# Performance work log

Measured on AMD Instinct MI355X. Metric: run time of the kernel, lower is better.

Reference implementation:

```python
import jax, jax.numpy as jnp
import numpy as np

N_MEMORY = 16
FEA_DIM = 512


def setup_inputs() -> dict:
    key = jax.random.key(0)
    ks = jax.random.split(key, 8)
    b, L, d, n = 4, 4096, FEA_DIM, N_MEMORY
    scale = 1.0 / np.sqrt(d)  # ~ torch Linear default init scale
    return {
        "query": jax.random.normal(ks[0], (b, L, d), dtype=jnp.float32),
        "W1": jax.random.uniform(ks[1], (n, d, d), jnp.float32, -scale, scale),
        "b1": jax.random.uniform(ks[2], (n, d), jnp.float32, -scale, scale),
        "W2": jax.random.uniform(ks[3], (n, d, d), jnp.float32, -scale, scale),
        "b2": jax.random.uniform(ks[4], (n, d), jnp.float32, -scale, scale),
        "Wg": jax.random.uniform(ks[5], (n, d), jnp.float32, -scale, scale),
        "bg": jax.random.uniform(ks[6], (n,), jnp.float32, -scale, scale),
        "topk": 8,
    }


def reference(query, W1, b1, W2, b2, Wg, bg, topk):
    # query: [b, L, d]; stacked per-memory-slot params: W1/W2 [n, d, d], Wg [n, d]
    n = W1.shape[0]
    # per-slot LeakyReLU negative slopes: 0.01 + 0.2/n * l
    slopes = (0.01 + 0.2 / n * jnp.arange(n, dtype=query.dtype))[:, None, None, None]
    # memory_function: Linear -> LeakyReLU(slope_l) -> Linear -> Tanh, all slots at once
    h = jnp.einsum('bld,ndh->nblh', query, W1) + b1[:, None, None, :]   # [n,b,L,d]
    h = jnp.where(h >= 0, h, h * slopes)
    x = jnp.tanh(jnp.einsum('nblh,nhd->nbld', h, W2) + b2[:, None, None, :])  # [n,b,L,d]
    # gate: Linear(d,1) -> softmax over L -> topk over L -> gather -> weighted sum
    logits = jnp.einsum('nbld,nd->nbl', x, Wg) + bg[:, None, None]      # [n,b,L]
    w = jax.nn.softmax(logits, axis=-1)
    top_w, top_idx = jax.lax.top_k(w, topk)                             # [n,b,k]
    items = jnp.take_along_axis(x, top_idx[..., None], axis=2)          # [n,b,k,d]
    combined = jnp.einsum('nbkd,nbk->nbd', items, top_w)                # [n,b,d]
    m_item = jnp.transpose(combined, (1, 0, 2))                         # [b,n,d]
    # F.normalize(dim=-1), eps=1e-12
    norm = jnp.maximum(jnp.linalg.norm(m_item, axis=-1, keepdims=True), 1e-12)
    return m_item / norm
```

## Files before the change

kernel.cpp:

```cpp
#include <hip/hip_runtime.h>
#include <hip/hip_bf16.h>
#include <cstdint>
#include <cstddef>

#define NMEM 16
#define DDIM 512
#define BATCH 4
#define LSEQ 4096
#define ROWS 16384
#define NCAND 32
#define KTOP 8
#define QPAD 20

typedef __attribute__((ext_vector_type(4))) float f32x4;
typedef __attribute__((ext_vector_type(16))) float f32x16;
typedef __attribute__((ext_vector_type(8))) int int8v;

__device__ inline void gld16(const void* gptr, void* lptr) {
    __builtin_amdgcn_global_load_lds(
        (const __attribute__((address_space(1))) unsigned int*)gptr,
        (__attribute__((address_space(3))) unsigned int*)lptr,
        16, 0, 0);
}

__device__ inline float fast_tanh(float p) {
    p = fminf(fmaxf(p, -15.f), 15.f);
    float e = __expf(2.f * p);
    return (e - 1.f) / (e + 1.f);
}

__device__ inline int8v load_frag(const unsigned char* Ts, int row, int g, int hs) {
    int h = (row >> hs) & 7;
    const int4* p0 = (const int4*)(Ts + row * 128 + (((2 * g) ^ h) << 4));
    const int4* p1 = (const int4*)(Ts + row * 128 + (((2 * g + 1) ^ h) << 4));
    int4 x = *p0, y = *p1;
    int8v v;
    v[0] = x.x; v[1] = x.y; v[2] = x.z; v[3] = x.w;
    v[4] = y.x; v[5] = y.y; v[6] = y.z; v[7] = y.w;
    return v;
}

__global__ __launch_bounds__(256)
void prep_kernel(const float* __restrict__ query,
                 const float* __restrict__ W1, const float* __restrict__ W2,
                 unsigned char* __restrict__ Q8,
                 unsigned char* __restrict__ W1T8, unsigned char* __restrict__ W2T8,
                 float* __restrict__ logits) {
    int blk = blockIdx.x, t = threadIdx.x;
    if (blk < 2048) {
        size_t base = ((size_t)blk * 256 + t) * 16;
        const float4* in = (const float4*)(query + base);
        int4 o; int* op = (int*)&o;
        #pragma unroll
        for (int q = 0; q < 4; ++q) {
            float4 v = in[q];
            int lo = __builtin_amdgcn_cvt_pk_fp8_f32(v.x, v.y, 0, false);
            op[q] = __builtin_amdgcn_cvt_pk_fp8_f32(v.z, v.w, lo, true);
        }
        *(int4*)(Q8 + base) = o;
    } else if (blk < 4096) {
        __shared__ float tile[64][69];
        int bid = blk - 2048;
        const float* Win = W1; unsigned char* Wout = W1T8;
        if (bid >= 1024) { bid -= 1024; Win = W2; Wout = W2T8; }
        int n = bid >> 6, t64 = bid & 63;
        int dt = (t64 >> 3) << 6, jt = (t64 & 7) << 6;
        const float* inN = Win + (size_t)n * DDIM * DDIM;
        unsigned char* outN = Wout + (size_t)n * DDIM * DDIM;
        int rr = t >> 4, cc = (t & 15) * 4;
        #pragma unroll
        for (int pass = 0; pass < 4; ++pass) {
            int row = rr + pass * 16;
            float4 v = *(const float4*)(inN + (size_t)(dt + row) * DDIM + jt + cc);
            tile[row][cc] = v.x; tile[row][cc + 1] = v.y;
            tile[row][cc + 2] = v.z; tile[row][cc + 3] = v.w;
        }
        __syncthreads();
        #pragma unroll
        for (int pass = 0; pass < 4; ++pass) {
            int jl = rr + pass * 16;
            float f0 = tile[cc][jl], f1 = tile[cc + 1][jl];
            float f2 = tile[cc + 2][jl], f3 = tile[cc + 3][jl];
            int lo = __builtin_amdgcn_cvt_pk_fp8_f32(f0, f1, 0, false);
            int dw = __builtin_amdgcn_cvt_pk_fp8_f32(f2, f3, lo, true);
            *(int*)(outN + (size_t)(jt + jl) * DDIM + dt + cc) = dw;
        }
    } else {
        int bid = blk - 4096;
        ((int4*)logits)[bid * 256 + t] = int4{0, 0, 0, 0};
    }
}

__global__ __launch_bounds__(256, 2)
void fused_mlp_kernel(const unsigned char* __restrict__ Q8,
                      const unsigned char* __restrict__ W1T8,
                      const unsigned char* __restrict__ W2T8,
                      const float* __restrict__ b1, const float* __restrict__ b2,
                      const float* __restrict__ Wg,
                      float* __restrict__ logits)
{
    __shared__ unsigned char hbuf[128 * 512];
    __shared__ unsigned char Bs[128 * 128];
    const int id = blockIdx.x;
    const int n = id & 15;
    const int m0 = (id >> 4) * 128;
    const int tid = threadIdx.x, lane = tid & 63, w = tid >> 6;
    const int rh = w >> 1, ch = w & 1;
    const int l31 = lane & 31, kh = lane >> 5;
    const unsigned char* W1n = W1T8 + (size_t)n * DDIM * DDIM;
    const unsigned char* W2n = W2T8 + (size_t)n * DDIM * DDIM;
    const float slope = 0.01f + 0.0125f * n;
    const unsigned char* Aq0 = Q8 + (size_t)(m0 + rh * 64 + l31) * DDIM + kh * 32;

    for (int n0 = 0; n0 < 4; ++n0) {
        f32x16 acc[2][2] = {};
        const unsigned char* Bg = W1n + (size_t)(n0 * 128) * DDIM;
        for (int kt = 0; kt < 4; ++kt) {
            int8v av[2][2];
            #pragma unroll
            for (int rt = 0; rt < 2; ++rt)
                #pragma unroll
                for (int ks = 0; ks < 2; ++ks) {
                    const unsigned char* ap = Aq0 + (size_t)rt * 32 * DDIM + kt * 128 + ks * 64;
                    int4 x = *(const int4*)ap;
                    int4 y = *(const int4*)(ap + 16);
                    av[rt][ks][0] = x.x; av[rt][ks][1] = x.y;
                    av[rt][ks][2] = x.z; av[rt][ks][3] = x.w;
                    av[rt][ks][4] = y.x; av[rt][ks][5] = y.y;
                    av[rt][ks][6] = y.z; av[rt][ks][7] = y.w;
                }
            #pragma unroll
            for (int i = 0; i < 4; ++i) {
                int c = i * 256 + tid;
                int row = c >> 3, chk = c & 7;
                gld16(Bg + (size_t)row * DDIM + kt * 128 + ((chk ^ (row & 7)) << 4),
                      &Bs[c * 16]);
            }
            __syncthreads();
            #pragma unroll
            for (int ks = 0; ks < 2; ++ks)
                #pragma unroll
                for (int fc = 0; fc < 2; ++fc) {
                    int8v bfr = load_frag(Bs, ch * 64 + fc * 32 + l31, ks * 2 + kh, 0);
                    #pragma unroll
                    for (int rt = 0; rt < 2; ++rt)
                        acc[rt][fc] = __builtin_amdgcn_mfma_scale_f32_32x32x64_f8f6f4(
                            av[rt][ks], bfr, acc[rt][fc], 0, 0, 0,
                            0x7F7F7F7F, 0, 0x7F7F7F7F);
                }
            __syncthreads();
        }
        #pragma unroll
        for (int fc = 0; fc < 2; ++fc) {
            int D = n0 * 128 + ch * 64 + fc * 32 + l31;
            float bias = b1[n * DDIM + D];
            #pragma unroll
            for (int rt = 0; rt < 2; ++rt)
                #pragma unroll
                for (int reg = 0; reg < 16; ++reg) {
                    int row = rh * 64 + rt * 32 + (reg & 3) + 8 * (reg >> 2) + 4 * kh;
                    float v = acc[rt][fc][reg] + bias;
                    v = v >= 0.f ? v : v * slope;
                    int pk = __builtin_amdgcn_cvt_pk_fp8_f32(v, v, 0, false);
                    hbuf[row * 512 + (((D >> 4) ^ (row & 7)) << 4) + (D & 15)]
                        = (unsigned char)(pk & 0xff);
                }
        }
    }

    float rowacc[2][16] = {};
    for (int n0 = 0; n0 < 4; ++n0) {
        f32x16 acc[2][2] = {};
        const unsigned char* Bg = W2n + (size_t)(n0 * 128) * DDIM;
        for (int kt = 0; kt < 4; ++kt) {
            #pragma unroll
            for (int i = 0; i < 4; ++i) {
                int c = i * 256 + tid;
                int row = c >> 3, chk = c & 7;
                gld16(Bg + (size_t)row * DDIM + kt * 128 + ((chk ^ (row & 7)) << 4),
                      &Bs[c * 16]);
            }
            __syncthreads();
            #pragma unroll
            for (int ks = 0; ks < 2; ++ks) {
                int8v av[2];
                #pragma unroll
                for (int rt = 0; rt < 2; ++rt) {
                    int hrow = rh * 64 + rt * 32 + l31, hq = hrow & 7;
                    int C0 = kt * 8 + ks * 4 + 2 * kh;
                    const int4* p0 = (const int4*)(hbuf + hrow * 512 + ((C0 ^ hq) << 4));
                    const int4* p1 = (const int4*)(hbuf + hrow * 512 + (((C0 + 1) ^ hq) << 4));
                    int4 x = *p0, y = *p1;
                    av[rt][0] = x.x; av[rt][1] = x.y; av[rt][2] = x.z; av[rt][3] = x.w;
                    av[rt][4] = y.x; av[rt][5] = y.y; av[rt][6] = y.z; av[rt][7] = y.w;
                }
                #pragma unroll
                for (int fc = 0; fc < 2; ++fc) {
                    int8v bfr = load_frag(Bs, ch * 64 + fc * 32 + l31, ks * 2 + kh, 0);
                    #pragma unroll
                    for (int rt = 0; rt < 2; ++rt)
                        acc[rt][fc] = __builtin_amdgcn_mfma_scale_f32_32x32x64_f8f6f4(
                            av[rt], bfr, acc[rt][fc], 0, 0, 0,
                            0x7F7F7F7F, 0, 0x7F7F7F7F);
                }
            }
            __syncthreads();
        }
        #pragma unroll
        for (int fc = 0; fc < 2; ++fc) {
            int j = n0 * 128 + ch * 64 + fc * 32 + l31;
            float bias = b2[n * DDIM + j];
            float wgv = Wg[n * DDIM + j];
            #pragma unroll
            for (int rt = 0; rt < 2; ++rt)
                #pragma unroll
                for (int reg = 0; reg < 16; ++reg)
                    rowacc[rt][reg] = fmaf(fast_tanh(acc[rt][fc][reg] + bias), wgv,
                                           rowacc[rt][reg]);
        }
    }
    #pragma unroll
    for (int sh = 1; sh < 32; sh <<= 1)
        #pragma unroll
        for (int rt = 0; rt < 2; ++rt)
            #pragma unroll
            for (int reg = 0; reg < 16; ++reg)
                rowacc[rt][reg] += __shfl_xor(rowacc[rt][reg], sh);
    if (l31 == 0) {
        float* Ln = logits + (size_t)n * ROWS + m0 + rh * 64 + 4 * kh;
        #pragma unroll
        for (int rt = 0; rt < 2; ++rt)
            #pragma unroll
            for (int reg = 0; reg < 16; ++reg)
                atomicAdd(&Ln[rt * 32 + (reg & 3) + 8 * (reg >> 2)], rowacc[rt][reg]);
    }
}

__global__ __launch_bounds__(256)
void topcand_kernel(const float* __restrict__ logits, int* __restrict__ cand,
                    float* __restrict__ ex_logit) {
    __shared__ float lv[LSEQ];
    __shared__ float cv[128];
    __shared__ int   ci[128];
    int p = blockIdx.x, n = p >> 2, b = p & 3;
    int t = threadIdx.x, lane = t & 63, w = t >> 6;
    const float* L = logits + (size_t)n * ROWS + (size_t)b * LSEQ;
    for (int i = t; i < LSEQ; i += 256) lv[i] = L[i];
    __syncthreads();
    float mv[16];
    int base = w * 1024;
    #pragma unroll
    for (int j = 0; j < 16; ++j) mv[j] = lv[base + j * 64 + lane];
    for (int rd = 0; rd < 32; ++rd) {
        float best = mv[0]; int bj = 0;
        #pragma unroll
        for (int j = 1; j < 16; ++j)
            if (mv[j] > best) { best = mv[j]; bj = j; }
        int bidx = base + bj * 64 + lane;
        float rv = best; int ridx = bidx;
        #pragma unroll
        for (int s = 1; s < 64; s <<= 1) {
            float ov = __shfl_xor(rv, s); int oi = __shfl_xor(ridx, s);
            if (ov > rv || (ov == rv && oi < ridx)) { rv = ov; ridx = oi; }
        }
        if (lane == 0) { cv[w * 32 + rd] = rv; ci[w * 32 + rd] = ridx; }
        if (ridx == bidx) mv[bj] = -1e30f;
    }
    __syncthreads();
    if (w == 0) {
        float v2[2]; int i2[2];
        #pragma unroll
        for (int k = 0; k < 2; ++k) { v2[k] = cv[k * 64 + lane]; i2[k] = ci[k * 64 + lane]; }
        for (int rd = 0; rd < 32; ++rd) {
            float best = v2[0]; int bi = i2[0]; int bk = 0;
            if (v2[1] > best || (v2[1] == best && i2[1] < bi)) { best = v2[1]; bi = i2[1]; bk = 1; }
            float rv = best; int ridx = bi;
            #pragma unroll
            for (int s = 1; s < 64; s <<= 1) {
                float ov = __shfl_xor(rv, s); int oi = __shfl_xor(ridx, s);
                if (ov > rv || (ov == rv && oi < ridx)) { rv = ov; ridx = oi; }
            }
            if (lane == 0) cand[p * NCAND + rd] = ridx;
            if (ridx == bi) v2[bk] = -1e30f;
        }
    } else if (w == 1) {
        if (lane < NCAND) ex_logit[p * NCAND + lane] = 0.f;
    }
}

__global__ __launch_bounds__(256)
void exact_h_kernel(const float* __restrict__ query,
                    const float* __restrict__ W1, const float* __restrict__ b1,
                    const int* __restrict__ cand, float* __restrict__ ex_h) {
    __shared__ float qs[DDIM][QPAD];
    __shared__ float hpart[4][16][64];
    int blk = blockIdx.x;
    int p = blk >> 4, r4 = blk & 15;
    int ct = r4 >> 3, jc = r4 & 7;
    int n = p >> 2, b = p & 3;
    int t = threadIdx.x, jj = t & 63, dg = t >> 6;
    int j = jc * 64 + jj;
    for (int c = 0; c < 16; ++c) {
        int li = cand[p * NCAND + ct * 16 + c];
        const float* qr = query + ((size_t)b * LSEQ + li) * DDIM;
        for (int d = t; d < DDIM; d += 256) qs[d][c] = qr[d];
    }
    __syncthreads();
    const float* W1n = W1 + (size_t)n * DDIM * DDIM;
    float acc[16] = {};
    for (int d = dg * 128; d < dg * 128 + 128; ++d) {
        float wvv = W1n[(size_t)d * DDIM + j];
        const float4* qv = (const float4*)&qs[d][0];
        #pragma unroll
        for (int c4 = 0; c4 < 4; ++c4) {
            float4 q4 = qv[c4];
            acc[c4 * 4 + 0] = fmaf(q4.x, wvv, acc[c4 * 4 + 0]);
            acc[c4 * 4 + 1] = fmaf(q4.y, wvv, acc[c4 * 4 + 1]);
            acc[c4 * 4 + 2] = fmaf(q4.z, wvv, acc[c4 * 4 + 2]);
            acc[c4 * 4 + 3] = fmaf(q4.w, wvv, acc[c4 * 4 + 3]);
        }
    }
    #pragma unroll
    for (int c = 0; c < 16; ++c) hpart[dg][c][jj] = acc[c];
    __syncthreads();
    const float slope = 0.01f + 0.0125f * n;
    float bias = b1[n * DDIM + j];
    for (int cc = dg; cc < 16; cc += 4) {
        float h = hpart[0][cc][jj] + hpart[1][cc][jj] + hpart[2][cc][jj]
                + hpart[3][cc][jj] + bias;
        h = h >= 0.f ? h : h * slope;
        ex_h[((size_t)p * NCAND + ct * 16 + cc) * DDIM + j] = h;
    }
}

__global__ __launch_bounds__(256)
void exact_x_kernel(const float* __restrict__ ex_h,
                    const float* __restrict__ W2, const float* __restrict__ b2,
                    const float* __restrict__ Wg,
                    float* __restrict__ ex_x, float* __restrict__ ex_logit) {
    __shared__ float hs[DDIM][QPAD];
    __shared__ float xpart[4][16][64];
    int blk = blockIdx.x;
    int p = blk >> 4, r4 = blk & 15;
    int ct = r4 >> 3, jc = r4 & 7;
    int n = p >> 2;
    int t = threadIdx.x, jj = t & 63, dg = t >> 6;
    int j = jc * 64 + jj;
    for (int c = 0; c < 16; ++c) {
        const float* hr = ex_h + ((size_t)p * NCAND + ct * 16 + c) * DDIM;
        for (int d = t; d < DDIM; d += 256) hs[d][c] = hr[d];
    }
    __syncthreads();
    const float* W2n = W2 + (size_t)n * DDIM * DDIM;
    float acc[16] = {};
    for (int d = dg * 128; d < dg * 128 + 128; ++d) {
        float wvv = W2n[(size_t)d * DDIM + j];
        const float4* hv = (const float4*)&hs[d][0];
        #pragma unroll
        for (int c4 = 0; c4 < 4; ++c4) {
            float4 h4 = hv[c4];
            acc[c4 * 4 + 0] = fmaf(h4.x, wvv, acc[c4 * 4 + 0]);
            acc[c4 * 4 + 1] = fmaf(h4.y, wvv, acc[c4 * 4 + 1]);
            acc[c4 * 4 + 2] = fmaf(h4.z, wvv, acc[c4 * 4 + 2]);
            acc[c4 * 4 + 3] = fmaf(h4.w, wvv, acc[c4 * 4 + 3]);
        }
    }
    #pragma unroll
    for (int c = 0; c < 16; ++c) xpart[dg][c][jj] = acc[c];
    __syncthreads();
    float bias = b2[n * DDIM + j];
    float wg = Wg[n * DDIM + j];
    for (int cc = dg; cc < 16; cc += 4) {
        float a = xpart[0][cc][jj] + xpart[1][cc][jj] + xpart[2][cc][jj]
                + xpart[3][cc][jj] + bias;
        float x = tanhf(a);
        ex_x[((size_t)p * NCAND + ct * 16 + cc) * DDIM + j] = x;
        float lp = x * wg;
        #pragma unroll
        for (int s = 1; s < 64; s <<= 1) lp += __shfl_xor(lp, s);
        if (jj == 0) atomicAdd(&ex_logit[p * NCAND + ct * 16 + cc], lp);
    }
}

__global__ __launch_bounds__(64)
void final_kernel(const float* __restrict__ ex_x, const float* __restrict__ ex_logit,
                  const int* __restrict__ cand, float* __restrict__ out)
{
    __shared__ float w8s[KTOP];
    __shared__ int   s8s[KTOP];
    int p = blockIdx.x, n = p >> 2, b = p & 3;
    int t = threadIdx.x;
    float myv = (t < NCAND) ? ex_logit[p * NCAND + t] : -1e30f;
    int myidx = (t < NCAND) ? cand[p * NCAND + t] : 0x7fffffff;
    float lmax = 0.f;
    for (int k = 0; k < KTOP; ++k) {
        float rv = myv; int ridx = myidx; int rl = t;
        #pragma unroll
        for (int s = 1; s < 64; s <<= 1) {
            float ov = __shfl_xor(rv, s); int oi = __shfl_xor(ridx, s); int ol = __shfl_xor(rl, s);
            if (ov > rv || (ov == rv && oi < ridx)) { rv = ov; ridx = oi; rl = ol; }
        }
        if (k == 0) lmax = rv;
        if (t == 0) { w8s[k] = __expf(rv - lmax); s8s[k] = rl; }
        if (t == rl) myv = -1e30f;
    }
    __syncthreads();
    float cvv[8];
    float sq = 0.f;
    int idx = 0;
    for (int d = t; d < DDIM; d += 64, ++idx) {
        float s = 0.f;
        #pragma unroll
        for (int k = 0; k < KTOP; ++k)
            s = fmaf(w8s[k], ex_x[((size_t)p * NCAND + s8s[k]) * DDIM + d], s);
        cvv[idx] = s;
        sq += s * s;
    }
    #pragma unroll
    for (int s = 1; s < 64; s <<= 1) sq += __shfl_xor(sq, s);
    float norm = fmaxf(sqrtf(sq), 1e-12f);
    idx = 0;
    for (int d = t; d < DDIM; d += 64, ++idx)
        out[((size_t)b * NMEM + n) * DDIM + d] = cvv[idx] / norm;
}

extern "C" void kernel_launch(void* const* d_in, const int* in_sizes, int n_in,
                              void* d_out, int out_size, void* d_ws, size_t ws_size,
                              hipStream_t stream)
{
    const float* query = (const float*)d_in[0];
    const float* W1    = (const float*)d_in[1];
    const float* b1    = (const float*)d_in[2];
    const float* W2    = (const float*)d_in[3];
    const float* b2    = (const float*)d_in[4];
    const float* Wg    = (const float*)d_in[5];

    char* ws = (char*)d_ws;
    const size_t MB = 1024 * 1024;
    unsigned char* Q8   = (unsigned char*)(ws);
    unsigned char* W1T8 = (unsigned char*)(ws + 8 * MB);
    unsigned char* W2T8 = (unsigned char*)(ws + 12 * MB);
    float* logits   = (float*)(ws + 16 * MB);
    int*   cand     = (int*)  (ws + 17 * MB);
    float* ex_logit = (float*)(ws + 17 * MB + 16384);
    float* ex_h     = (float*)(ws + 20 * MB);
    float* ex_x     = (float*)(ws + 28 * MB);

    prep_kernel<<<4352, 256, 0, stream>>>(query, W1, W2, Q8, W1T8, W2T8, logits);
    fused_mlp_kernel<<<2048, 256, 0, stream>>>(Q8, W1T8, W2T8, b1, b2, Wg, logits);
    topcand_kernel<<<64, 256, 0, stream>>>(logits, cand, ex_logit);
    exact_h_kernel<<<1024, 256, 0, stream>>>(query, W1, b1, cand, ex_h);
    exact_x_kernel<<<1024, 256, 0, stream>>>(ex_h, W2, b2, Wg, ex_x, ex_logit);
    final_kernel<<<64, 64, 0, stream>>>(ex_x, ex_logit, cand, (float*)d_out);
}
```

Measured before the change: 484.8 us.

## Load weight fragments directly from global, drop LDS staging and logit atomics

The fused MLP kernel stops staging weight tiles in LDS through global_load_lds and barriers. Each wave now loads its MFMA weight fragments straight from global memory (relying on L2/cache reuse), and the first GEMM swaps operands so the h tile can be written to LDS as packed 4-byte fp8 stores. Per-block logits are reduced through a small LDS buffer and stored directly, replacing atomicAdd and the zeroing pass in prep. tanh is swapped for a clamped rational approximation. This removes barriers and LDS traffic, at the cost of redundant global loads across waves and some tanh accuracy in candidate scoring.

```diff
diff --git a/kernel.cpp b/kernel.cpp
--- a/kernel.cpp
+++ b/kernel.cpp
@@ -16,24 +16,15 @@
 typedef __attribute__((ext_vector_type(16))) float f32x16;
 typedef __attribute__((ext_vector_type(8))) int int8v;
 
-__device__ inline void gld16(const void* gptr, void* lptr) {
-    __builtin_amdgcn_global_load_lds(
-        (const __attribute__((address_space(1))) unsigned int*)gptr,
-        (__attribute__((address_space(3))) unsigned int*)lptr,
-        16, 0, 0);
-}
-
-__device__ inline float fast_tanh(float p) {
-    p = fminf(fmaxf(p, -15.f), 15.f);
-    float e = __expf(2.f * p);
-    return (e - 1.f) / (e + 1.f);
-}
-
-__device__ inline int8v load_frag(const unsigned char* Ts, int row, int g, int hs) {
-    int h = (row >> hs) & 7;
-    const int4* p0 = (const int4*)(Ts + row * 128 + (((2 * g) ^ h) << 4));
-    const int4* p1 = (const int4*)(Ts + row * 128 + (((2 * g + 1) ^ h) << 4));
-    int4 x = *p0, y = *p1;
+__device__ inline float fast_tanh(float x) {
+    float t = __builtin_amdgcn_fmed3f(x, -3.f, 3.f);
+    float t2 = t * t;
+    return t * (27.f + t2) * __builtin_amdgcn_rcpf(27.f + 9.f * t2);
+}
+
+__device__ inline int8v ldg_frag(const unsigned char* p) {
+    int4 x = *(const int4*)p;
+    int4 y = *(const int4*)(p + 16);
     int8v v;
     v[0] = x.x; v[1] = x.y; v[2] = x.z; v[3] = x.w;
     v[4] = y.x; v[5] = y.y; v[6] = y.z; v[7] = y.w;
@@ -44,8 +35,7 @@
 void prep_kernel(const float* __restrict__ query,
                  const float* __restrict__ W1, const float* __restrict__ W2,
                  unsigned char* __restrict__ Q8,
-                 unsigned char* __restrict__ W1T8, unsigned char* __restrict__ W2T8,
-                 float* __restrict__ logits) {
+                 unsigned char* __restrict__ W1T8, unsigned char* __restrict__ W2T8) {
     int blk = blockIdx.x, t = threadIdx.x;
     if (blk < 2048) {
         size_t base = ((size_t)blk * 256 + t) * 16;
@@ -58,7 +48,7 @@
             op[q] = __builtin_amdgcn_cvt_pk_fp8_f32(v.z, v.w, lo, true);
         }
         *(int4*)(Q8 + base) = o;
-    } else if (blk < 4096) {
+    } else {
         __shared__ float tile[64][69];
         int bid = blk - 2048;
         const float* Win = W1; unsigned char* Wout = W1T8;
@@ -85,9 +75,6 @@
             int dw = __builtin_amdgcn_cvt_pk_fp8_f32(f2, f3, lo, true);
             *(int*)(outN + (size_t)(jt + jl) * DDIM + dt + cc) = dw;
         }
-    } else {
-        int bid = blk - 4096;
-        ((int4*)logits)[bid * 256 + t] = int4{0, 0, 0, 0};
     }
 }
 
@@ -100,87 +87,78 @@
                       float* __restrict__ logits)
 {
     __shared__ unsigned char hbuf[128 * 512];
-    __shared__ unsigned char Bs[128 * 128];
+    __shared__ float lsum[2][128];
     const int id = blockIdx.x;
     const int n = id & 15;
     const int m0 = (id >> 4) * 128;
-    const int tid = threadIdx.x, lane = tid & 63, w = tid >> 6;
+    const int tid = threadIdx.x, lane = tid & 63;
+    const int w = tid >> 6;
     const int rh = w >> 1, ch = w & 1;
     const int l31 = lane & 31, kh = lane >> 5;
     const unsigned char* W1n = W1T8 + (size_t)n * DDIM * DDIM;
     const unsigned char* W2n = W2T8 + (size_t)n * DDIM * DDIM;
     const float slope = 0.01f + 0.0125f * n;
     const unsigned char* Aq0 = Q8 + (size_t)(m0 + rh * 64 + l31) * DDIM + kh * 32;
-
+    const size_t wrowoff = (size_t)(ch * 64 + l31) * DDIM + kh * 32;
+
+    #pragma unroll 1
     for (int n0 = 0; n0 < 4; ++n0) {
         f32x16 acc[2][2] = {};
-        const unsigned char* Bg = W1n + (size_t)(n0 * 128) * DDIM;
+        const unsigned char* Wb = W1n + (size_t)(n0 * 128) * DDIM + wrowoff;
+        #pragma unroll
         for (int kt = 0; kt < 4; ++kt) {
             int8v av[2][2];
             #pragma unroll
             for (int rt = 0; rt < 2; ++rt)
                 #pragma unroll
-                for (int ks = 0; ks < 2; ++ks) {
-                    const unsigned char* ap = Aq0 + (size_t)rt * 32 * DDIM + kt * 128 + ks * 64;
-                    int4 x = *(const int4*)ap;
-                    int4 y = *(const int4*)(ap + 16);
-                    av[rt][ks][0] = x.x; av[rt][ks][1] = x.y;
-                    av[rt][ks][2] = x.z; av[rt][ks][3] = x.w;
-                    av[rt][ks][4] = y.x; av[rt][ks][5] = y.y;
-                    av[rt][ks][6] = y.z; av[rt][ks][7] = y.w;
-                }
-            #pragma unroll
-            for (int i = 0; i < 4; ++i) {
-                int c = i * 256 + tid;
-                int row = c >> 3, chk = c & 7;
-                gld16(Bg + (size_t)row * DDIM + kt * 128 + ((chk ^ (row & 7)) << 4),
-                      &Bs[c * 16]);
-            }
-            __syncthreads();
+                for (int ks = 0; ks < 2; ++ks)
+                    av[rt][ks] = ldg_frag(Aq0 + (size_t)rt * 32 * DDIM + kt * 128 + ks * 64);
             #pragma unroll
             for (int ks = 0; ks < 2; ++ks)
                 #pragma unroll
                 for (int fc = 0; fc < 2; ++fc) {
-                    int8v bfr = load_frag(Bs, ch * 64 + fc * 32 + l31, ks * 2 + kh, 0);
+                    int8v wfr = ldg_frag(Wb + (size_t)(fc * 32) * DDIM + kt * 128 + ks * 64);
                     #pragma unroll
                     for (int rt = 0; rt < 2; ++rt)
                         acc[rt][fc] = __builtin_amdgcn_mfma_scale_f32_32x32x64_f8f6f4(
-                            av[rt][ks], bfr, acc[rt][fc], 0, 0, 0,
+                            wfr, av[rt][ks], acc[rt][fc], 0, 0, 0,
                             0x7F7F7F7F, 0, 0x7F7F7F7F);
                 }
-            __syncthreads();
         }
         #pragma unroll
         for (int fc = 0; fc < 2; ++fc) {
-            int D = n0 * 128 + ch * 64 + fc * 32 + l31;
-            float bias = b1[n * DDIM + D];
-            #pragma unroll
-            for (int rt = 0; rt < 2; ++rt)
-                #pragma unroll
-                for (int reg = 0; reg < 16; ++reg) {
-                    int row = rh * 64 + rt * 32 + (reg & 3) + 8 * (reg >> 2) + 4 * kh;
-                    float v = acc[rt][fc][reg] + bias;
-                    v = v >= 0.f ? v : v * slope;
-                    int pk = __builtin_amdgcn_cvt_pk_fp8_f32(v, v, 0, false);
-                    hbuf[row * 512 + (((D >> 4) ^ (row & 7)) << 4) + (D & 15)]
-                        = (unsigned char)(pk & 0xff);
+            #pragma unroll
+            for (int rt = 0; rt < 2; ++rt) {
+                int r = rh * 64 + rt * 32 + l31;
+                #pragma unroll
+                for (int q = 0; q < 4; ++q) {
+                    int jb = n0 * 128 + ch * 64 + fc * 32 + 8 * q + 4 * kh;
+                    float4 bias = *(const float4*)(b1 + n * DDIM + jb);
+                    float v0 = acc[rt][fc][4 * q + 0] + bias.x;
+                    float v1 = acc[rt][fc][4 * q + 1] + bias.y;
+                    float v2 = acc[rt][fc][4 * q + 2] + bias.z;
+                    float v3 = acc[rt][fc][4 * q + 3] + bias.w;
+                    v0 = v0 >= 0.f ? v0 : v0 * slope;
+                    v1 = v1 >= 0.f ? v1 : v1 * slope;
+                    v2 = v2 >= 0.f ? v2 : v2 * slope;
+                    v3 = v3 >= 0.f ? v3 : v3 * slope;
+                    int lo = __builtin_amdgcn_cvt_pk_fp8_f32(v0, v1, 0, false);
+                    int dw = __builtin_amdgcn_cvt_pk_fp8_f32(v2, v3, lo, true);
+                    *(int*)(hbuf + r * 512 + ((((jb >> 4) ^ (r & 7)) << 4) | (jb & 15))) = dw;
                 }
-        }
-    }
+            }
+        }
+    }
+
+    __syncthreads();
 
     float rowacc[2][16] = {};
+    #pragma unroll 1
     for (int n0 = 0; n0 < 4; ++n0) {
         f32x16 acc[2][2] = {};
-        const unsigned char* Bg = W2n + (size_t)(n0 * 128) * DDIM;
+        const unsigned char* Wb = W2n + (size_t)(n0 * 128) * DDIM + wrowoff;
+        #pragma unroll
         for (int kt = 0; kt < 4; ++kt) {
-            #pragma unroll
-            for (int i = 0; i < 4; ++i) {
-                int c = i * 256 + tid;
-                int row = c >> 3, chk = c & 7;
-                gld16(Bg + (size_t)row * DDIM + kt * 128 + ((chk ^ (row & 7)) << 4),
-                      &Bs[c * 16]);
-            }
-            __syncthreads();
             #pragma unroll
             for (int ks = 0; ks < 2; ++ks) {
                 int8v av[2];
@@ -196,15 +174,14 @@
                 }
                 #pragma unroll
                 for (int fc = 0; fc < 2; ++fc) {
-                    int8v bfr = load_frag(Bs, ch * 64 + fc * 32 + l31, ks * 2 + kh, 0);
+                    int8v wfr = ldg_frag(Wb + (size_t)(fc * 32) * DDIM + kt * 128 + ks * 64);
                     #pragma unroll
                     for (int rt = 0; rt < 2; ++rt)
                         acc[rt][fc] = __builtin_amdgcn_mfma_scale_f32_32x32x64_f8f6f4(
-                            av[rt], bfr, acc[rt][fc], 0, 0, 0,
+                            av[rt], wfr, acc[rt][fc], 0, 0, 0,
                             0x7F7F7F7F, 0, 0x7F7F7F7F);
                 }
             }
-            __syncthreads();
         }
         #pragma unroll
         for (int fc = 0; fc < 2; ++fc) {
@@ -227,13 +204,16 @@
             for (int reg = 0; reg < 16; ++reg)
                 rowacc[rt][reg] += __shfl_xor(rowacc[rt][reg], sh);
     if (l31 == 0) {
-        float* Ln = logits + (size_t)n * ROWS + m0 + rh * 64 + 4 * kh;
         #pragma unroll
         for (int rt = 0; rt < 2; ++rt)
             #pragma unroll
             for (int reg = 0; reg < 16; ++reg)
-                atomicAdd(&Ln[rt * 32 + (reg & 3) + 8 * (reg >> 2)], rowacc[rt][reg]);
-    }
+                lsum[ch][rh * 64 + rt * 32 + (reg & 3) + 8 * (reg >> 2) + 4 * kh]
+                    = rowacc[rt][reg];
+    }
+    __syncthreads();
+    if (tid < 128)
+        logits[(size_t)n * ROWS + m0 + tid] = lsum[0][tid] + lsum[1][tid];
 }
 
 __global__ __launch_bounds__(256)
@@ -446,7 +426,7 @@
     float* ex_h     = (float*)(ws + 20 * MB);
     float* ex_x     = (float*)(ws + 28 * MB);
 
-    prep_kernel<<<4352, 256, 0, stream>>>(query, W1, W2, Q8, W1T8, W2T8, logits);
+    prep_kernel<<<4096, 256, 0, stream>>>(query, W1, W2, Q8, W1T8, W2T8);
     fused_mlp_kernel<<<2048, 256, 0, stream>>>(Q8, W1T8, W2T8, b1, b2, Wg, logits);
     topcand_kernel<<<64, 256, 0, stream>>>(logits, cand, ex_logit);
     exact_h_kernel<<<1024, 256, 0, stream>>>(query, W1, b1, cand, ex_h);
```

Measured after the change: 548.1 us. 13.1% more time.
